# Kernel optimization log

Hardware: AMD Instinct MI355X
Metric: run time of the kernel (lower is better)

## Reference

```python
import jax, jax.numpy as jnp
import numpy as np

D_MODEL, D_STATE, D_CONV, EXPAND = 1024, 16, 4, 2
D_INNER = EXPAND * D_MODEL          # 2048
DT_RANK = -(-D_MODEL // 16)        # 64
B_SZ, SEQ = 4, 2048


def setup_inputs() -> dict:
    key = jax.random.key(0)
    ks = jax.random.split(key, 10)
    s = 0.02
    x = jax.random.normal(ks[0], (B_SZ, SEQ, D_MODEL), jnp.float32)
    in_proj_w = s * jax.random.normal(ks[1], (2, 2 * D_INNER, D_MODEL), jnp.float32)
    conv_w = s * jax.random.normal(ks[2], (2, D_INNER, D_CONV), jnp.float32)
    conv_b = s * jax.random.normal(ks[3], (2, D_INNER), jnp.float32)
    x_proj_w = s * jax.random.normal(ks[4], (2, DT_RANK + 2 * D_STATE, D_INNER), jnp.float32)
    dt_proj_w = s * jax.random.normal(ks[5], (2, D_INNER, DT_RANK), jnp.float32)
    # bias chosen so softplus(dt) is small and the scan is stable (mamba-style dt init)
    dt_proj_b = jax.random.uniform(ks[6], (2, D_INNER), jnp.float32, -5.0, -3.0)
    # A_log = log(A) with A in [1, d_state], per real Mamba init (S4D-real)
    A_log = jnp.log(jax.random.uniform(ks[7], (2, D_INNER, D_STATE), jnp.float32, 1.0, float(D_STATE)))
    D_param = jnp.ones((2, D_INNER), jnp.float32) + s * jax.random.normal(ks[8], (2, D_INNER), jnp.float32)
    out_proj_w = s * jax.random.normal(ks[9], (2, D_MODEL, D_INNER), jnp.float32)
    return {"x": x, "in_proj_w": in_proj_w, "conv_w": conv_w, "conv_b": conv_b,
            "x_proj_w": x_proj_w, "dt_proj_w": dt_proj_w, "dt_proj_b": dt_proj_b,
            "A_log": A_log, "D_param": D_param, "out_proj_w": out_proj_w}


def _mamba(x, in_w, cw, cb, xw, dtw, dtb, A_log, Dp, ow):
    """Single-direction Mamba forward. x: [B, L, d_model]."""
    B, L, _ = x.shape
    xz = jnp.einsum('bld,ed->ble', x, in_w)          # [B, L, 2*d_inner]
    xi, z = jnp.split(xz, 2, axis=-1)
    # depthwise causal conv1d over time, kernel d_conv
    xp = jnp.pad(xi, ((0, 0), (D_CONV - 1, 0), (0, 0)))
    xc = cb + sum(cw[:, k] * xp[:, k:k + L, :] for k in range(D_CONV))
    xc = jax.nn.silu(xc)                              # [B, L, d_inner]
    proj = jnp.einsum('bld,ed->ble', xc, xw)          # [B, L, dt_rank+2*d_state]
    dt_raw, Bm, Cm = jnp.split(proj, [DT_RANK, DT_RANK + D_STATE], axis=-1)
    dt = jax.nn.softplus(jnp.einsum('blr,dr->bld', dt_raw, dtw) + dtb)  # [B, L, d_inner]
    A = -jnp.exp(A_log)                               # [d_inner, d_state]

    def step(h, inp):
        dt_t, B_t, C_t, x_t = inp                     # [B,d_inner],[B,S],[B,S],[B,d_inner]
        dA = jnp.exp(dt_t[..., None] * A)             # [B, d_inner, d_state]
        h = h * dA + (dt_t * x_t)[..., None] * B_t[:, None, :]
        y = jnp.einsum('bds,bs->bd', h, C_t)
        return h, y

    h0 = jnp.zeros((B, D_INNER, D_STATE), x.dtype)
    inps = (dt.transpose(1, 0, 2), Bm.transpose(1, 0, 2),
            Cm.transpose(1, 0, 2), xc.transpose(1, 0, 2))
    _, ys = jax.lax.scan(step, h0, inps)              # ys: [L, B, d_inner]
    y = ys.transpose(1, 0, 2) + xc * Dp
    y = y * jax.nn.silu(z)
    return jnp.einsum('bld,md->blm', y, ow)           # [B, L, d_model]


def reference(x, in_proj_w, conv_w, conv_b, x_proj_w, dt_proj_w, dt_proj_b, A_log, D_param, out_proj_w):
    y_f = _mamba(x, in_proj_w[0], conv_w[0], conv_b[0], x_proj_w[0],
                 dt_proj_w[0], dt_proj_b[0], A_log[0], D_param[0], out_proj_w[0])
    xb = jnp.flip(x, axis=1)
    y_b = _mamba(xb, in_proj_w[1], conv_w[1], conv_b[1], x_proj_w[1],
                 dt_proj_w[1], dt_proj_b[1], A_log[1], D_param[1], out_proj_w[1])
    return y_f + jnp.flip(y_b, axis=1)
```

## Files before the change

### kernel.cpp

```cpp
#include <hip/hip_runtime.h>
#include <hip/hip_bf16.h>
#include <math.h>
#include <stdio.h>


using u16 = unsigned short;
using u32 = unsigned int;

typedef __bf16 bf16x8 __attribute__((ext_vector_type(8)));
typedef float  f32x4  __attribute__((ext_vector_type(4)));
typedef u32    u32x4  __attribute__((ext_vector_type(4)));
typedef u16    u16x4  __attribute__((ext_vector_type(4)));

#define DEVINL __device__ __forceinline__

DEVINL float b2f(u16 u) { union { u32 i; float f; } v; v.i = ((u32)u) << 16; return v.f; }
DEVINL u16 f2b(float f) {
  union { float f; u32 i; } v; v.f = f;
  u32 i = v.i;
  return (u16)((i + 0x7FFFu + ((i >> 16) & 1u)) >> 16);
}

#define L2E 1.4426950408889634f
#define LN2 0.6931471805599453f

DEVINL float fast_silu(float a) {
  const float e = __builtin_amdgcn_exp2f(-a * L2E);
  return a * __builtin_amdgcn_rcpf(1.f + e);
}
DEVINL float fast_softplus(float x) {
  if (x > 20.f) return x;
  return LN2 * __builtin_amdgcn_logf(1.f + __builtin_amdgcn_exp2f(x * L2E));
}

DEVINL void gl_lds16(const u16* g, u16* l) {
  __builtin_amdgcn_global_load_lds(
      (__attribute__((address_space(1))) void*)const_cast<u16*>(g),
      (__attribute__((address_space(3))) void*)l, 16, 0, 0);
}

#define BAR()    asm volatile("s_barrier" ::: "memory")
#define LGKM(N)  asm volatile("s_waitcnt lgkmcnt(" #N ")" ::: "memory")
#define VM0()    asm volatile("s_waitcnt vmcnt(0)" ::: "memory")
#define SCHB()   __builtin_amdgcn_sched_barrier(0)
#define NOPS     ((void)0)

__global__ __launch_bounds__(512, 2) void k_gemm256(
    const u16* __restrict__ A, int lda, int flipA,
    const u16* __restrict__ Bw, int ldb,
    u16* __restrict__ C, int ldc, int K)
{
  extern __shared__ __align__(16) char lds[];

  const int tid  = threadIdx.x;
  const int lane = tid & 63;
  const int wid  = tid >> 6;

  const int mBase = blockIdx.x * 256;
  const int nBase = blockIdx.y * 256;

  const int rloc = lane >> 3;
  const int scol = ((lane & 7) ^ rloc) << 3;
  const u16* srcA[2][2];
  const u16* srcB[2][2];
#pragma unroll
  for (int h = 0; h < 2; ++h)
#pragma unroll
    for (int i = 0; i < 2; ++i) {
      int ra = mBase + h * 128 + wid * 16 + i * 8 + rloc;
      if (flipA) ra ^= 2047;
      const int rb = nBase + h * 128 + wid * 16 + i * 8 + rloc;
      srcA[h][i] = A  + (long long)ra * lda + scol;
      srcB[h][i] = Bw + (long long)rb * ldb + scol;
    }
  u16* const dA = (u16*)lds + wid * 1024;
  u16* const dB = (u16*)lds + 32768 + wid * 1024;

  const int lhi16 = (lane >> 4) * 16;
  const int swz   = (lane & 7) << 4;
  const int rdA   = ((wid >> 2) * 64 + (lane & 15)) * 128 + (lhi16 ^ swz);
  const int rdAx  = rdA ^ 64;
  const int rdB   = 65536 + ((wid & 3) * 32 + (lane & 15)) * 128 + (lhi16 ^ swz);
  const int rdBx  = rdB ^ 64;

  f32x4 acc[2][2][4][2];
#pragma unroll
  for (int a = 0; a < 2; ++a)
#pragma unroll
    for (int b = 0; b < 2; ++b)
#pragma unroll
      for (int c = 0; c < 4; ++c)
#pragma unroll
        for (int d = 0; d < 2; ++d) acc[a][b][c][d] = (f32x4){0.f, 0.f, 0.f, 0.f};

  bf16x8 af[4][2], bq0[2][2], bq1[2][2];

#define LDSV(off) (*(const bf16x8*)(lds + (off)))
#define READ_A(CB, QM, DST) do {                                               \
  _Pragma("unroll") for (int fm = 0; fm < 4; ++fm) {                           \
    DST[fm][0] = LDSV((CB)*32768 + (QM)*16384 + fm*2048 + rdA);                \
    DST[fm][1] = LDSV((CB)*32768 + (QM)*16384 + fm*2048 + rdAx); }             \
} while (0)
#define READ_B(CB, QN, DST) do {                                               \
  _Pragma("unroll") for (int fn = 0; fn < 2; ++fn) {                           \
    DST[fn][0] = LDSV((CB)*32768 + (QN)*16384 + fn*2048 + rdB);                \
    DST[fn][1] = LDSV((CB)*32768 + (QN)*16384 + fn*2048 + rdBx); }             \
} while (0)
#define MMA(QM, QN, AF, BFR) do {                                              \
  __builtin_amdgcn_s_setprio(1);                                              \
  _Pragma("unroll") for (int fm = 0; fm < 4; ++fm)                             \
  _Pragma("unroll") for (int fn = 0; fn < 2; ++fn)                             \
  _Pragma("unroll") for (int kk = 0; kk < 2; ++kk)                             \
    acc[QM][QN][fm][fn] = __builtin_amdgcn_mfma_f32_16x16x32_bf16(             \
        AF[fm][kk], BFR[fn][kk], acc[QM][QN][fm][fn], 0, 0, 0);                \
  __builtin_amdgcn_s_setprio(0);                                              \
} while (0)
#define STAGE_ALL(CB, KT) do {                                                 \
  gl_lds16(srcA[0][0] + (KT)*64, dA + (CB)*16384);                             \
  gl_lds16(srcA[0][1] + (KT)*64, dA + (CB)*16384 + 512);                       \
  gl_lds16(srcA[1][0] + (KT)*64, dA + (CB)*16384 + 8192);                      \
  gl_lds16(srcA[1][1] + (KT)*64, dA + (CB)*16384 + 8192 + 512);                \
  gl_lds16(srcB[0][0] + (KT)*64, dB + (CB)*16384);                             \
  gl_lds16(srcB[0][1] + (KT)*64, dB + (CB)*16384 + 512);                       \
  gl_lds16(srcB[1][0] + (KT)*64, dB + (CB)*16384 + 8192);                      \
  gl_lds16(srcB[1][1] + (KT)*64, dB + (CB)*16384 + 8192 + 512);                \
} while (0)

#define KTILE2(CB, STG) do {                                                   \
  STG;                                                                         \
  READ_A(CB, 0, af); READ_B(CB, 0, bq0); READ_B(CB, 1, bq1);                   \
  LGKM(4); SCHB();                                                             \
  MMA(0, 0, af, bq0);                                                          \
  LGKM(0); SCHB();                                                             \
  MMA(0, 1, af, bq1);                                                          \
  READ_A(CB, 1, af);                                                           \
  LGKM(0); SCHB();                                                             \
  MMA(1, 1, af, bq1);                                                          \
  MMA(1, 0, af, bq0);                                                          \
  VM0(); BAR();                                                                \
} while (0)

  STAGE_ALL(0, 0);
  VM0(); BAR();

  for (int it = 0; it < 7; ++it) {
    const int kt = 2 * it;
    KTILE2(0, STAGE_ALL(1, kt + 1));
    KTILE2(1, STAGE_ALL(0, kt + 2));
  }
  KTILE2(0, STAGE_ALL(1, 15));
  KTILE2(1, NOPS);

  const int rq = (lane >> 4) << 2;
  const int cn = lane & 15;
  const long long mW = mBase + (wid >> 2) * 64;
  const int nW = nBase + (wid & 3) * 32;
#pragma unroll
  for (int qm = 0; qm < 2; ++qm)
#pragma unroll
    for (int qn = 0; qn < 2; ++qn)
#pragma unroll
      for (int fm = 0; fm < 4; ++fm)
#pragma unroll
        for (int fn = 0; fn < 2; ++fn)
#pragma unroll
          for (int r = 0; r < 4; ++r) {
            const long long m = mW + qm * 128 + fm * 16 + rq + r;
            const int n = nW + qn * 128 + fn * 16 + cn;
            C[m * ldc + n] = f2b(acc[qm][qn][fm][fn][r]);
          }
#undef LDSV
#undef READ_A
#undef READ_B
#undef MMA
#undef STAGE_ALL
#undef KTILE2
}

template <int MODE>
__global__ __launch_bounds__(256) void k_gemm(
    const u16* __restrict__ A, int lda, int flipA,
    const u16* __restrict__ Bw, int ldb,
    void* __restrict__ Cout, int ldc, int K,
    float* __restrict__ f1, float* __restrict__ f2,
    float* __restrict__ out2)
{
  __shared__ __align__(16) u16 As[128 * 64];
  __shared__ __align__(16) u16 Bs[128 * 64];

  const int tid  = threadIdx.x;
  const int lane = tid & 63;
  const int wid  = tid >> 6;

  const int mBase = blockIdx.x * 128;
  const int nBase = blockIdx.y * 128;

  f32x4 acc[4][4];
#pragma unroll
  for (int i = 0; i < 4; ++i)
#pragma unroll
    for (int j = 0; j < 4; ++j) acc[i][j] = (f32x4){0.f, 0.f, 0.f, 0.f};

  const int wm = (wid & 1) * 64;
  const int wn = (wid >> 1) * 64;
  const int lrow = lane & 15;
  const int lk   = (lane >> 4) * 8;
  const int sr = tid >> 3;
  const int sc = (tid & 7) * 8;

  for (int k0 = 0; k0 < K; k0 += 64) {
#pragma unroll
    for (int i = 0; i < 4; ++i) {
      int ra = mBase + i * 32 + sr;
      if (flipA) ra ^= 2047;
      const int rb = nBase + i * 32 + sr;
      u16* la = &As[(i * 256 + wid * 64) * 8];
      u16* lb = &Bs[(i * 256 + wid * 64) * 8];
      gl_lds16(A  + (long long)ra * lda + (k0 + sc), la);
      gl_lds16(Bw + (long long)rb * ldb + (k0 + sc), lb);
    }
    __syncthreads();
#pragma unroll
    for (int kk = 0; kk < 64; kk += 32) {
      bf16x8 af[4], bfr[4];
#pragma unroll
      for (int f = 0; f < 4; ++f) {
        af[f]  = *(const bf16x8*)&As[(wm + f * 16 + lrow) * 64 + kk + lk];
        bfr[f] = *(const bf16x8*)&Bs[(wn + f * 16 + lrow) * 64 + kk + lk];
      }
#pragma unroll
      for (int fm = 0; fm < 4; ++fm)
#pragma unroll
        for (int fn = 0; fn < 4; ++fn)
          acc[fm][fn] = __builtin_amdgcn_mfma_f32_16x16x32_bf16(af[fm], bfr[fn], acc[fm][fn], 0, 0, 0);
    }
    __syncthreads();
  }

  const int rowq = (lane >> 4) * 4;
  const int coln = lane & 15;
#pragma unroll
  for (int fm = 0; fm < 4; ++fm) {
#pragma unroll
    for (int fn = 0; fn < 4; ++fn) {
#pragma unroll
      for (int r = 0; r < 4; ++r) {
        const long long m = mBase + wm + fm * 16 + rowq + r;
        const long long n = nBase + wn + fn * 16 + coln;
        const float v = acc[fm][fn][r];
        if constexpr (MODE == 0) {
          ((u16*)Cout)[m * ldc + n] = f2b(v);
        } else if constexpr (MODE == 1) {
          ((u16*)Cout)[m * ldc + n] = f2b(fast_softplus(v + f1[(int)n]));
        } else if constexpr (MODE == 2) {
          ((float*)Cout)[m * ldc + n] = v;
        } else if constexpr (MODE == 3) {
          const long long mf = m ^ 2047;
          out2[mf * ldc + n] = v + f2[mf * ldc + n];
        } else {
          if (n < 64)       ((u16*)Cout)[m * ldc + n] = f2b(v);
          else if (n < 80)  f1[m * 16 + (n - 64)] = v;
          else if (n < 96)  f2[m * 16 + (n - 80)] = v;
        }
      }
    }
  }
}

__global__ __launch_bounds__(256) void k_prep(
    const float* __restrict__ inw_d, u16* __restrict__ inwB,
    const float* __restrict__ xpw_d, u16* __restrict__ xw_pad,
    const float* __restrict__ dtw_d, u16* __restrict__ dtwB,
    const float* __restrict__ alog_d, float* __restrict__ A2,
    const float* __restrict__ cw_d, float* __restrict__ cwT)
{
  const int bx = blockIdx.x;
  const int tid = threadIdx.x;
  if (bx < 4096) {
    const int i = bx * 256 + tid;
    const f32x4 v = ((const f32x4*)inw_d)[i];
    u16x4 o = {f2b(v[0]), f2b(v[1]), f2b(v[2]), f2b(v[3])};
    ((u16x4*)inwB)[i] = o;
  } else if (bx < 5120) {
    const int idx = (bx - 4096) * 256 + tid;
    const int c = idx & 2047, r = idx >> 11;
    xw_pad[idx] = (r < 96) ? f2b(xpw_d[r * 2048 + c]) : (u16)0;
  } else if (bx < 5248) {
    const int i = (bx - 5120) * 256 + tid;
    const f32x4 v = ((const f32x4*)dtw_d)[i];
    u16x4 o = {f2b(v[0]), f2b(v[1]), f2b(v[2]), f2b(v[3])};
    ((u16x4*)dtwB)[i] = o;
  } else if (bx < 5376) {
    const int idx = (bx - 5248) * 256 + tid;
    A2[idx] = -expf(alog_d[idx]) * L2E;
  } else {
    const int idx = (bx - 5376) * 256 + tid;
    const int d = idx & 2047, k = idx >> 11;
    cwT[k * 2048 + d] = cw_d[d * 4 + k];
  }
}

__global__ __launch_bounds__(256) void k_castw(const float* __restrict__ src,
                                               u16* __restrict__ dst) {
  const int i = blockIdx.x * 256 + threadIdx.x;
  const f32x4 v = ((const f32x4*)src)[i];
  u16x4 o = {f2b(v[0]), f2b(v[1]), f2b(v[2]), f2b(v[3])};
  ((u16x4*)dst)[i] = o;
}

__global__ __launch_bounds__(256) void k_cast_x(const float* __restrict__ x,
                                                u16* __restrict__ xA) {
  const int idx = blockIdx.x * 256 + threadIdx.x;
  const f32x4 v = ((const f32x4*)x)[idx];
  u16x4 o = {f2b(v[0]), f2b(v[1]), f2b(v[2]), f2b(v[3])};
  ((u16x4*)xA)[idx] = o;
}

__global__ __launch_bounds__(256) void k_conv(const u16* __restrict__ xz,
                                              const float* __restrict__ cwT,
                                              const float* __restrict__ cb,
                                              u16* __restrict__ xc) {
  const int idx = blockIdx.x * 256 + threadIdx.x;
  const int d8  = idx & 255;
  const int gr  = idx >> 8;
  const int t   = gr & 2047;
  const int d0  = d8 * 8;

  float acc[8];
  {
    const f32x4 b0 = *(const f32x4*)(cb + d0);
    const f32x4 b1 = *(const f32x4*)(cb + d0 + 4);
#pragma unroll
    for (int j = 0; j < 4; ++j) { acc[j] = b0[j]; acc[4 + j] = b1[j]; }
  }

#pragma unroll
  for (int k = 0; k < 4; ++k) {
    const int tt = t - 3 + k;
    if (tt < 0) continue;
    const u32x4 v = *(const u32x4*)(xz + (long long)(gr + k - 3) * 4096 + d0);
    const u16* pv = (const u16*)&v;
    const f32x4 w0 = *(const f32x4*)(cwT + k * 2048 + d0);
    const f32x4 w1 = *(const f32x4*)(cwT + k * 2048 + d0 + 4);
#pragma unroll
    for (int j = 0; j < 4; ++j) {
      acc[j]     = fmaf(w0[j], b2f(pv[j]), acc[j]);
      acc[4 + j] = fmaf(w1[j], b2f(pv[4 + j]), acc[4 + j]);
    }
  }
  u16 o[8];
#pragma unroll
  for (int j = 0; j < 8; ++j) {
    o[j] = f2b(fast_silu(acc[j]));
  }
  *(u32x4*)(xc + (long long)gr * 2048 + d0) = *(const u32x4*)o;
}

__global__ __launch_bounds__(256) void k_scanA(
    const u16* __restrict__ dt, const u16* __restrict__ xc,
    const float* __restrict__ Bf, const float* __restrict__ A2,
    float* __restrict__ hbuf, float* __restrict__ sumdt)
{
  const int tid = threadIdx.x;
  const int bx  = blockIdx.x;
  const int d     = (bx & 7) * 256 + tid;
  const int chunk = (bx >> 3) & 31;
  const int b     = bx >> 8;

  float a2[16];
#pragma unroll
  for (int s = 0; s < 16; ++s) a2[s] = A2[d * 16 + s];

  float h[16];
#pragma unroll
  for (int s = 0; s < 16; ++s) h[s] = 0.f;
  float sdt = 0.f;

  const long long rowBase = (long long)b * 2048 + chunk * 64;
  for (int t0 = 0; t0 < 64; ++t0) {
    const long long gr = rowBase + t0;
    const float dtv = b2f(dt[gr * 2048 + d]);
    const float xcv = b2f(xc[gr * 2048 + d]);
    sdt += dtv;
    const float dtx = dtv * xcv;
    float Bv[16];
    *(f32x4*)&Bv[0]  = *(const f32x4*)(Bf + gr * 16);
    *(f32x4*)&Bv[4]  = *(const f32x4*)(Bf + gr * 16 + 4);
    *(f32x4*)&Bv[8]  = *(const f32x4*)(Bf + gr * 16 + 8);
    *(f32x4*)&Bv[12] = *(const f32x4*)(Bf + gr * 16 + 12);
#pragma unroll
    for (int s = 0; s < 16; ++s) {
      const float dA = __builtin_amdgcn_exp2f(a2[s] * dtv);
      h[s] = fmaf(h[s], dA, dtx * Bv[s]);
    }
  }
  const long long cbi = (long long)b * 32 + chunk;
#pragma unroll
  for (int s = 0; s < 16; ++s) hbuf[(cbi * 16 + s) * 2048 + d] = h[s];
  sumdt[cbi * 2048 + d] = sdt;
}

__global__ __launch_bounds__(256) void k_scanB(
    const float* __restrict__ A2, float* __restrict__ hbuf,
    const float* __restrict__ sumdt)
{
  const int tid = threadIdx.x;
  const int bx  = blockIdx.x;
  const int d   = (bx & 7) * 256 + tid;
  const int sg  = ((bx >> 3) & 1) * 8;
  const int b   = bx >> 4;

  float a2[8];
#pragma unroll
  for (int s = 0; s < 8; ++s) a2[s] = A2[d * 16 + sg + s];
  float h[8];
#pragma unroll
  for (int s = 0; s < 8; ++s) h[s] = 0.f;

  const long long base = (long long)b * 32;
  for (int c = 0; c < 32; ++c) {
    const long long cbi = base + c;
    const float sd = sumdt[cbi * 2048 + d];
#pragma unroll
    for (int s = 0; s < 8; ++s) {
      float* p = &hbuf[(cbi * 16 + sg + s) * 2048 + d];
      const float loc = *p;
      *p = h[s];
      const float P = __builtin_amdgcn_exp2f(a2[s] * sd);
      h[s] = fmaf(h[s], P, loc);
    }
  }
}

__global__ __launch_bounds__(256) void k_scanC(
    const u16* __restrict__ dt, const u16* __restrict__ xc,
    const float* __restrict__ Bf, const float* __restrict__ Cf,
    const float* __restrict__ A2, const float* __restrict__ hbuf,
    const float* __restrict__ Dp, u16* __restrict__ yz)
{
  const int tid = threadIdx.x;
  const int bx  = blockIdx.x;
  const int d     = (bx & 7) * 256 + tid;
  const int chunk = (bx >> 3) & 31;
  const int b     = bx >> 8;
  const float dp  = Dp[d];

  float a2[16];
#pragma unroll
  for (int s = 0; s < 16; ++s) a2[s] = A2[d * 16 + s];

  const long long cbi = (long long)b * 32 + chunk;
  float h[16];
#pragma unroll
  for (int s = 0; s < 16; ++s) h[s] = hbuf[(cbi * 16 + s) * 2048 + d];

  const long long rowBase = (long long)b * 2048 + chunk * 64;
  for (int t0 = 0; t0 < 64; ++t0) {
    const long long gr = rowBase + t0;
    const float dtv = b2f(dt[gr * 2048 + d]);
    const float xcv = b2f(xc[gr * 2048 + d]);
    const float dtx = dtv * xcv;
    float Bv[16], Cv[16];
    *(f32x4*)&Bv[0]  = *(const f32x4*)(Bf + gr * 16);
    *(f32x4*)&Bv[4]  = *(const f32x4*)(Bf + gr * 16 + 4);
    *(f32x4*)&Bv[8]  = *(const f32x4*)(Bf + gr * 16 + 8);
    *(f32x4*)&Bv[12] = *(const f32x4*)(Bf + gr * 16 + 12);
    *(f32x4*)&Cv[0]  = *(const f32x4*)(Cf + gr * 16);
    *(f32x4*)&Cv[4]  = *(const f32x4*)(Cf + gr * 16 + 4);
    *(f32x4*)&Cv[8]  = *(const f32x4*)(Cf + gr * 16 + 8);
    *(f32x4*)&Cv[12] = *(const f32x4*)(Cf + gr * 16 + 12);
    float y = 0.f;
#pragma unroll
    for (int s = 0; s < 16; ++s) {
      const float dA = __builtin_amdgcn_exp2f(a2[s] * dtv);
      h[s] = fmaf(h[s], dA, dtx * Bv[s]);
      y = fmaf(h[s], Cv[s], y);
    }
    const float z = b2f(yz[gr * 4096 + 2048 + d]);
    const float yv = (y + xcv * dp) * fast_silu(z);
    yz[gr * 4096 + d] = f2b(yv);
  }
}

extern "C" void kernel_launch(void* const* d_in, const int* in_sizes, int n_in,
                              void* d_out, int out_size, void* d_ws, size_t ws_size,
                              hipStream_t stream) {
  const float* x    = (const float*)d_in[0];
  const float* inw  = (const float*)d_in[1];
  const float* cw   = (const float*)d_in[2];
  const float* cb   = (const float*)d_in[3];
  const float* xpw  = (const float*)d_in[4];
  const float* dtw  = (const float*)d_in[5];
  const float* dtb  = (const float*)d_in[6];
  const float* alog = (const float*)d_in[7];
  const float* Dp   = (const float*)d_in[8];
  const float* ow   = (const float*)d_in[9];
  float* out = (float*)d_out;

  char* ws = (char*)d_ws;
  float* outacc = (float*)(ws + 0);
  u16*   xz_d   = (u16*)(ws + 33554432);
  u16*   xc_d   = (u16*)(ws + 100663296);
  u16*   inwB   = (u16*)(ws + 100663296);
  u16*   dt_d   = (u16*)(ws + 134217728);
  u16*   owB    = (u16*)(ws + 134217728);
  u16*   xA     = (u16*)(ws + 167772160);
  u16*   proj_d = (u16*)(ws + 184549376);
  u16*   xw_pad = (u16*)(ws + 185597952);
  float* A2     = (float*)(ws + 186122240);
  float* Bf     = (float*)(ws + 186253312);
  float* Cf     = (float*)(ws + 186777600);
  float* hbuf   = (float*)(ws + 187301888);
  float* sumdt  = (float*)(ws + 204079104);
  u16*   dtwB   = (u16*)(ws + 205127680);
  float* cwT    = (float*)(ws + 205389824);
  const size_t NEED = 205422592;

  (void)in_sizes; (void)n_in; (void)out_size;
  if (ws_size < NEED) {
    fprintf(stderr, "[BiMamba] ws_size=%zu < needed %zu — aborting launch\n", ws_size, NEED);
    return;
  }

  static bool attr_set = false;
  if (!attr_set) {
    (void)hipFuncSetAttribute((const void*)k_gemm256,
                              hipFuncAttributeMaxDynamicSharedMemorySize, 131072);
    attr_set = true;
  }

  k_cast_x<<<8192, 256, 0, stream>>>(x, xA);

  for (int dir = 0; dir < 2; ++dir) {
    const float* inw_d = inw + (long long)dir * 4096 * 1024;
    const float* cw_d  = cw  + dir * 2048 * 4;
    const float* cb_d  = cb  + dir * 2048;
    const float* xpw_d = xpw + dir * 96 * 2048;
    const float* dtw_d = dtw + dir * 2048 * 64;
    const float* dtb_d = dtb + dir * 2048;
    const float* al_d  = alog + dir * 2048 * 16;
    const float* Dp_d  = Dp  + dir * 2048;
    const float* ow_d  = ow  + (long long)dir * 1024 * 2048;

    k_prep<<<5408, 256, 0, stream>>>(inw_d, inwB, xpw_d, xw_pad,
                                     dtw_d, dtwB, al_d, A2, cw_d, cwT);

    k_gemm256<<<dim3(32, 16), 512, 131072, stream>>>(
        xA, 1024, dir, inwB, 1024, xz_d, 4096, 1024);

    k_conv<<<8192, 256, 0, stream>>>(xz_d, cwT, cb_d, xc_d);

    k_gemm<4><<<dim3(64, 1), 256, 0, stream>>>(
        xc_d, 2048, 0, xw_pad, 2048, proj_d, 64, 2048, Bf, Cf, nullptr);

    k_gemm<1><<<dim3(64, 16), 256, 0, stream>>>(
        proj_d, 64, 0, dtwB, 64, dt_d, 2048, 64,
        const_cast<float*>(dtb_d), nullptr, nullptr);

    k_scanA<<<1024, 256, 0, stream>>>(dt_d, xc_d, Bf, A2, hbuf, sumdt);
    k_scanB<<<64, 256, 0, stream>>>(A2, hbuf, sumdt);
    k_scanC<<<1024, 256, 0, stream>>>(dt_d, xc_d, Bf, Cf, A2, hbuf, Dp_d, xz_d);

    k_castw<<<2048, 256, 0, stream>>>(ow_d, owB);

    if (dir == 0) {
      k_gemm<2><<<dim3(64, 8), 256, 0, stream>>>(
          xz_d, 4096, 0, owB, 2048, outacc, 1024, 2048, nullptr, nullptr, nullptr);
    } else {
      k_gemm<3><<<dim3(64, 8), 256, 0, stream>>>(
          xz_d, 4096, 0, owB, 2048, nullptr, 1024, 2048,
          nullptr, outacc, out);
    }
  }
}
```

Baseline: 787.3 us.

## Add dedicated 256x128 tile out-projection GEMM with 8 waves and double buffering

```diff
diff --git a/kernel.cpp b/kernel.cpp
--- a/kernel.cpp
+++ b/kernel.cpp
@@ -175,6 +175,121 @@
 #undef MMA
 #undef STAGE_ALL
 #undef KTILE2
+}
+
+template <int MODE>
+__global__ __launch_bounds__(512, 2) void k_gemmOut(
+    const u16* __restrict__ A, int lda,
+    const u16* __restrict__ Bw, int ldb,
+    float* __restrict__ Cout, int ldc,
+    const float* __restrict__ f2, float* __restrict__ out2)
+{
+  extern __shared__ __align__(16) char lds[];
+
+  const int tid  = threadIdx.x;
+  const int lane = tid & 63;
+  const int wid  = tid >> 6;
+
+  const int mBase = blockIdx.x * 256;
+  const int nBase = blockIdx.y * 128;
+
+  const int rloc = lane >> 3;
+  const int scol = ((lane & 7) ^ rloc) << 3;
+  const u16* srcA[4];
+  const u16* srcB[2];
+#pragma unroll
+  for (int i = 0; i < 4; ++i)
+    srcA[i] = A + (long long)(mBase + i * 64 + wid * 8 + rloc) * lda + scol;
+#pragma unroll
+  for (int i = 0; i < 2; ++i)
+    srcB[i] = Bw + (long long)(nBase + i * 64 + wid * 8 + rloc) * ldb + scol;
+  u16* const dA = (u16*)lds + wid * 512;
+  u16* const dB = (u16*)lds + 32768 + wid * 512;
+
+  const int lhi16 = (lane >> 4) * 16;
+  const int swz   = (lane & 7) << 4;
+  const int rdA   = ((wid >> 1) * 64 + (lane & 15)) * 128 + (lhi16 ^ swz);
+  const int rdAx  = rdA ^ 64;
+  const int rdB   = 65536 + ((wid & 1) * 64 + (lane & 15)) * 128 + (lhi16 ^ swz);
+  const int rdBx  = rdB ^ 64;
+
+  f32x4 acc[4][4];
+#pragma unroll
+  for (int i = 0; i < 4; ++i)
+#pragma unroll
+    for (int j = 0; j < 4; ++j) acc[i][j] = (f32x4){0.f, 0.f, 0.f, 0.f};
+
+  bf16x8 af[4][2], bfr[4][2];
+
+#define LDSV(off) (*(const bf16x8*)(lds + (off)))
+#define RD_A(CB) do {                                                          \
+  _Pragma("unroll") for (int fm = 0; fm < 4; ++fm) {                           \
+    af[fm][0] = LDSV((CB)*32768 + fm*2048 + rdA);                              \
+    af[fm][1] = LDSV((CB)*32768 + fm*2048 + rdAx); }                           \
+} while (0)
+#define RD_B(CB) do {                                                          \
+  _Pragma("unroll") for (int fn = 0; fn < 4; ++fn) {                           \
+    bfr[fn][0] = LDSV((CB)*16384 + fn*2048 + rdB);                             \
+    bfr[fn][1] = LDSV((CB)*16384 + fn*2048 + rdBx); }                          \
+} while (0)
+#define STG_ALL(CB, KT) do {                                                   \
+  gl_lds16(srcA[0] + (KT)*64, dA + (CB)*16384);                                \
+  gl_lds16(srcA[1] + (KT)*64, dA + (CB)*16384 + 4096);                         \
+  gl_lds16(srcA[2] + (KT)*64, dA + (CB)*16384 + 8192);                         \
+  gl_lds16(srcA[3] + (KT)*64, dA + (CB)*16384 + 12288);                        \
+  gl_lds16(srcB[0] + (KT)*64, dB + (CB)*8192);                                 \
+  gl_lds16(srcB[1] + (KT)*64, dB + (CB)*8192 + 4096);                          \
+} while (0)
+#define KTILE3(CB, STG) do {                                                   \
+  STG;                                                                         \
+  RD_A(CB); RD_B(CB);                                                          \
+  LGKM(0); SCHB();                                                             \
+  __builtin_amdgcn_s_setprio(1);                                              \
+  _Pragma("unroll") for (int fm = 0; fm < 4; ++fm)                             \
+  _Pragma("unroll") for (int fn = 0; fn < 4; ++fn)                             \
+  _Pragma("unroll") for (int kk = 0; kk < 2; ++kk)                             \
+    acc[fm][fn] = __builtin_amdgcn_mfma_f32_16x16x32_bf16(                     \
+        af[fm][kk], bfr[fn][kk], acc[fm][fn], 0, 0, 0);                        \
+  __builtin_amdgcn_s_setprio(0);                                              \
+  VM0(); BAR();                                                                \
+} while (0)
+
+  STG_ALL(0, 0);
+  VM0(); BAR();
+
+  for (int it = 0; it < 15; ++it) {
+    const int kt = 2 * it;
+    KTILE3(0, STG_ALL(1, kt + 1));
+    KTILE3(1, STG_ALL(0, kt + 2));
+  }
+  KTILE3(0, STG_ALL(1, 31));
+  KTILE3(1, NOPS);
+
+  const int rq = (lane >> 4) << 2;
+  const int cn = lane & 15;
+  const long long mW = mBase + (wid >> 1) * 64;
+  const int nW = nBase + (wid & 1) * 64;
+#pragma unroll
+  for (int fm = 0; fm < 4; ++fm)
+#pragma unroll
+    for (int fn = 0; fn < 4; ++fn)
+#pragma unroll
+      for (int r = 0; r < 4; ++r) {
+        const long long m = mW + fm * 16 + rq + r;
+        const int n = nW + fn * 16 + cn;
+        const float v = acc[fm][fn][r];
+        if constexpr (MODE == 2) {
+          Cout[m * ldc + n] = v;
+        } else {
+          const long long mf = m ^ 2047;
+          out2[mf * ldc + n] = v + f2[mf * ldc + n];
+        }
+      }
+#undef LDSV
+#undef RD_A
+#undef RD_B
+#undef STG_ALL
+#undef KTILE3
 }
 
 template <int MODE>
@@ -526,6 +641,10 @@
   if (!attr_set) {
     (void)hipFuncSetAttribute((const void*)k_gemm256,
                               hipFuncAttributeMaxDynamicSharedMemorySize, 131072);
+    (void)hipFuncSetAttribute((const void*)k_gemmOut<2>,
+                              hipFuncAttributeMaxDynamicSharedMemorySize, 98304);
+    (void)hipFuncSetAttribute((const void*)k_gemmOut<3>,
+                              hipFuncAttributeMaxDynamicSharedMemorySize, 98304);
     attr_set = true;
   }
 
@@ -564,12 +683,11 @@
     k_castw<<<2048, 256, 0, stream>>>(ow_d, owB);
 
     if (dir == 0) {
-      k_gemm<2><<<dim3(64, 8), 256, 0, stream>>>(
-          xz_d, 4096, 0, owB, 2048, outacc, 1024, 2048, nullptr, nullptr, nullptr);
+      k_gemmOut<2><<<dim3(32, 8), 512, 98304, stream>>>(
+          xz_d, 4096, owB, 2048, outacc, 1024, nullptr, nullptr);
     } else {
-      k_gemm<3><<<dim3(64, 8), 256, 0, stream>>>(
-          xz_d, 4096, 0, owB, 2048, nullptr, 1024, 2048,
-          nullptr, outacc, out);
-    }
-  }
-}
+      k_gemmOut<3><<<dim3(32, 8), 512, 98304, stream>>>(
+          xz_d, 4096, owB, 2048, nullptr, 1024, outacc, out);
+    }
+  }
+}
```

Result: faster. 741.4 us (-5.8%).
